# Performance work log

Measured on AMD Instinct MI355X. Metric: run time of the kernel, lower is better.

The kernel has to match this reference:

```python
import jax, jax.numpy as jnp
import numpy as np

HEAD_NUM = 8
EMB = 256
HEAD_SIZE = EMB // HEAD_NUM
POS_LEN = 128
ROPE_BASE = 100.0
LN_EPS = 1e-5
SOFTPICK_EPS = 1e-6


def _rope_tables():
    inv_freq = 1.0 / ROPE_BASE ** (jnp.arange(0, HEAD_SIZE, 2, dtype=jnp.float32) / HEAD_SIZE)
    t = jnp.arange(POS_LEN, dtype=jnp.float32)
    freqs = jnp.einsum('i,j->ij', t, inv_freq)          # [W, hs/2]
    freqs = jnp.concatenate([freqs, freqs], axis=-1)     # [W, hs]
    return jnp.sin(freqs), jnp.cos(freqs)


def _apply_rope(e, sin, cos):
    # e: [..., W, hs]; sin/cos: [W, hs]
    h = HEAD_SIZE // 2
    rot = jnp.concatenate([-e[..., h:], e[..., :h]], axis=-1)
    return e * cos + rot * sin


def _layernorm(x, g, b):
    mu = jnp.mean(x, axis=-1, keepdims=True)
    var = jnp.mean(jnp.square(x - mu), axis=-1, keepdims=True)
    return (x - mu) * jax.lax.rsqrt(var + LN_EPS) * g + b


def _softpick(x):
    m = jnp.max(x, axis=-1, keepdims=True)
    e = jnp.exp(x - m) - jnp.exp(-m)
    return jax.nn.relu(e) / (jnp.sum(jnp.abs(e), axis=-1, keepdims=True) + SOFTPICK_EPS)


def setup_inputs() -> dict:
    key = jax.random.key(0)
    ks = jax.random.split(key, 12)
    B, C, H, W = 4, EMB, 256, 128
    hn, hs = HEAD_NUM, HEAD_SIZE
    s = 0.02
    return {
        'left': jax.random.normal(ks[0], (B, C, H, W), jnp.float32),
        'right': jax.random.normal(ks[1], (B, C, H, W), jnp.float32),
        'qw': jax.random.normal(ks[2], (hn, hs, hs), jnp.float32) * s,   # grouped 1x1 conv weights
        'kw': jax.random.normal(ks[3], (hn, hs, hs), jnp.float32) * s,
        'vw': jax.random.normal(ks[4], (hn, hs, hs), jnp.float32) * s,
        'proj_w': jax.random.normal(ks[5], (C, C), jnp.float32) * s,
        'proj_b': jnp.zeros((C,), jnp.float32),
        'ln1_g': jnp.ones((C,), jnp.float32),
        'ln1_b': jnp.zeros((C,), jnp.float32),
        'ln2_g': jnp.ones((C,), jnp.float32),
        'ln2_b': jnp.zeros((C,), jnp.float32),
        'w1': jax.random.normal(ks[6], (C, 4 * C), jnp.float32) * s,
        'b1': jnp.zeros((4 * C,), jnp.float32),
        'w2': jax.random.normal(ks[7], (4 * C, C), jnp.float32) * s,
        'b2': jnp.zeros((C,), jnp.float32),
    }


def reference(left, right, qw, kw, vw, proj_w, proj_b,
              ln1_g, ln1_b, ln2_g, ln2_b, w1, b1, w2, b2):
    B, C, H, W = left.shape
    hn, hs = HEAD_NUM, HEAD_SIZE
    scale = hs ** -0.5
    sin, cos = _rope_tables()  # [W, hs]

    def grouped_proj(x, w):
        # grouped 1x1 conv -> per-head matmul; out [B, H, hn, W, hs]
        xr = x.reshape(B, hn, hs, H, W)
        return jnp.einsum('bgihw,goi->bhgwo', xr, w)

    q = _apply_rope(grouped_proj(left, qw), sin, cos)
    k = _apply_rope(grouped_proj(right, kw), sin, cos)
    v = grouped_proj(right, vw)

    att = _softpick(jnp.einsum('bhgqd,bhgkd->bhgqk', q, k) * scale)  # [B,H,hn,W,W]
    out = jnp.einsum('bhgqk,bhgkd->bhqgd', att, v).reshape(B, H, W, C)

    x1 = _layernorm(out @ proj_w + proj_b + jnp.transpose(left, (0, 2, 3, 1)), ln1_g, ln1_b)
    ffn = jax.nn.gelu(x1 @ w1 + b1, approximate=False) @ w2 + b2
    return _layernorm(ffn + x1, ln2_g, ln2_b)
```

## Files before the change

kernel.cpp:

```cpp
#include <hip/hip_runtime.h>
#include <hip/hip_bf16.h>

#define DEV __device__ __forceinline__

typedef __attribute__((ext_vector_type(8))) short bf16x8_t;
typedef __attribute__((ext_vector_type(4))) float f32x4_t;

constexpr int cB = 4, cC = 256, cH = 256, cW = 128, cHN = 8, cHS = 32;
constexpr int cM = cB * cH * cW;

DEV float bfu(unsigned int b16) { union { unsigned int u; float f; } v; v.u = b16 << 16; return v.f; }
DEV unsigned short f2bb(float f) { union { __hip_bfloat16 h; unsigned short u; } v; v.h = __float2bfloat16(f); return v.u; }
DEV unsigned int pk2(float a, float b) { return (unsigned)f2bb(a) | ((unsigned)f2bb(b) << 16); }

#define GLOAD_LDS16(g, l) \
  __builtin_amdgcn_global_load_lds((const __attribute__((address_space(1))) void*)(g), \
                                   (__attribute__((address_space(3))) void*)(l), 16, 0, 0)

DEV float gelu_fast(float v) {
  float ax = fabsf(v) * 0.7071067811865475f;
  float t = __builtin_amdgcn_rcpf(1.0f + 0.3275911f * ax);
  float poly = ((((1.061405429f * t - 1.453152027f) * t + 1.421413741f) * t
                 - 0.284496736f) * t + 0.254829592f) * t;
  float e = __expf(-ax * ax);
  float erfv = 1.0f - poly * e;
  float phi = 0.5f + 0.5f * copysignf(erfv, v);
  return v * phi;
}

__global__ __launch_bounds__(256) void transpose_bf16(const float* __restrict__ src,
                                                      __hip_bfloat16* __restrict__ dst,
                                                      int R, int Ccol) {
  int idx = blockIdx.x * 256 + threadIdx.x;
  if (idx < R * Ccol) {
    int r = idx / Ccol, c = idx - r * Ccol;
    dst[c * R + r] = __float2bfloat16(src[idx]);
  }
}

__global__ __launch_bounds__(256) void transpose_perm_bf16(const float* __restrict__ src,
                                                           __hip_bfloat16* __restrict__ dst,
                                                           int R, int Ccol) {
  int idx = blockIdx.x * 256 + threadIdx.x;
  if (idx < R * Ccol) {
    int r = idx / Ccol, c = idx - r * Ccol;
    int pk = (r & ~63) | ((r & 15) << 2) | ((r >> 4) & 3);
    dst[c * R + pk] = __float2bfloat16(src[idx]);
  }
}

__global__ __launch_bounds__(256) void rope_init(float2* __restrict__ tab) {
  int i = blockIdx.x * 256 + threadIdx.x;
  int w = i >> 4, c = i & 15;
  float inv = expf((float)c * -0.28782313662425572f);
  float ang = (float)w * inv;
  tab[i] = make_float2(sinf(ang), cosf(ang));
}

constexpr int XL_OFF = 0, XR_OFF = 10240, WQ_OFF = 20480, WK_OFF = 23040, WV_OFF = 25600;
constexpr int QS_OFF = 28160, KS_OFF = 38400, VT_OFF = 0, P_OFF = 10240;
constexpr int SMEM_BYTES = 48640;

__global__ __launch_bounds__(256) void attn_mfma(
    const float* __restrict__ left, const float* __restrict__ right,
    const float* __restrict__ qw, const float* __restrict__ kw, const float* __restrict__ vw,
    const float2* __restrict__ rope,
    __hip_bfloat16* __restrict__ att_out)
{
  __shared__ __align__(16) char smem[SMEM_BYTES];

  const int t = threadIdx.x;
  const int g = blockIdx.x & 7;
  const int h = (blockIdx.x >> 3) & 255;
  const int b = blockIdx.x >> 11;
  const size_t HW = (size_t)cH * cW;

  {
    const float* lb = left  + ((size_t)(b * cC + g * cHS) * cH + h) * cW;
    const float* rb = right + ((size_t)(b * cC + g * cHS) * cH + h) * cW;
    int w = t & 127, ih = (t >> 7) * 16;
    unsigned short* xlrow = (unsigned short*)(smem + XL_OFF) + w * 40 + ih;
    unsigned short* xrrow = (unsigned short*)(smem + XR_OFF) + w * 40 + ih;
#pragma unroll
    for (int i = 0; i < 16; i += 2) {
      float a0 = lb[(size_t)(ih + i) * HW + w], a1 = lb[(size_t)(ih + i + 1) * HW + w];
      *(unsigned int*)(xlrow + i) = pk2(a0, a1);
      float c0 = rb[(size_t)(ih + i) * HW + w], c1 = rb[(size_t)(ih + i + 1) * HW + w];
      *(unsigned int*)(xrrow + i) = pk2(c0, c1);
    }
    int o = t >> 3, i0 = (t & 7) * 4;
    {
      float4 v4 = *(const float4*)(qw + g * 1024 + t * 4);
      unsigned short* dst = (unsigned short*)(smem + WQ_OFF) + o * 40 + i0;
      *(unsigned int*)(dst) = pk2(v4.x, v4.y); *(unsigned int*)(dst + 2) = pk2(v4.z, v4.w);
    }
    {
      float4 v4 = *(const float4*)(kw + g * 1024 + t * 4);
      unsigned short* dst = (unsigned short*)(smem + WK_OFF) + o * 40 + i0;
      *(unsigned int*)(dst) = pk2(v4.x, v4.y); *(unsigned int*)(dst + 2) = pk2(v4.z, v4.w);
    }
    {
      float4 v4 = *(const float4*)(vw + g * 1024 + t * 4);
      unsigned short* dst = (unsigned short*)(smem + WV_OFF) + o * 40 + i0;
      *(unsigned int*)(dst) = pk2(v4.x, v4.y); *(unsigned int*)(dst + 2) = pk2(v4.z, v4.w);
    }
  }
  __syncthreads();

  const int lane = t & 63, wid = t >> 6;
  const int c = lane & 15, q4 = lane >> 4;
  const int wbase = wid * 32;
  const f32x4_t zero = {0.f, 0.f, 0.f, 0.f};

  bf16x8_t a_xl[2], a_xr[2];
#pragma unroll
  for (int sub = 0; sub < 2; ++sub) {
    a_xl[sub] = *(const bf16x8_t*)(smem + XL_OFF + (wbase + sub * 16 + c) * 80 + q4 * 16);
    a_xr[sub] = *(const bf16x8_t*)(smem + XR_OFF + (wbase + sub * 16 + c) * 80 + q4 * 16);
  }
  f32x4_t qacc[2][2], kacc[2][2];
#pragma unroll
  for (int ot = 0; ot < 2; ++ot) {
    bf16x8_t bq = *(const bf16x8_t*)(smem + WQ_OFF + (ot * 16 + c) * 80 + q4 * 16);
    bf16x8_t bk = *(const bf16x8_t*)(smem + WK_OFF + (ot * 16 + c) * 80 + q4 * 16);
#pragma unroll
    for (int sub = 0; sub < 2; ++sub) {
      qacc[sub][ot] = __builtin_amdgcn_mfma_f32_16x16x32_bf16(a_xl[sub], bq, zero, 0, 0, 0);
      kacc[sub][ot] = __builtin_amdgcn_mfma_f32_16x16x32_bf16(a_xr[sub], bk, zero, 0, 0, 0);
    }
  }
  {
    const float scale = 0.17677669529663687f;
    unsigned short* qsp = (unsigned short*)(smem + QS_OFF);
    unsigned short* ksp = (unsigned short*)(smem + KS_OFF);
#pragma unroll
    for (int sub = 0; sub < 2; ++sub)
#pragma unroll
      for (int r = 0; r < 4; ++r) {
        int w = wbase + sub * 16 + q4 * 4 + r;
        float2 sc = rope[w * 16 + c];
        float sn = sc.x, cs = sc.y;
        float q0 = qacc[sub][0][r], q1 = qacc[sub][1][r];
        qsp[w * 40 + c]      = f2bb((q0 * cs - q1 * sn) * scale);
        qsp[w * 40 + c + 16] = f2bb((q1 * cs + q0 * sn) * scale);
        float k0 = kacc[sub][0][r], k1 = kacc[sub][1][r];
        ksp[w * 40 + c]      = f2bb(k0 * cs - k1 * sn);
        ksp[w * 40 + c + 16] = f2bb(k1 * cs + k0 * sn);
      }
  }
  __syncthreads();

  {
    f32x4_t vacc[2][2];
#pragma unroll
    for (int dt = 0; dt < 2; ++dt) {
      bf16x8_t awv = *(const bf16x8_t*)(smem + WV_OFF + (dt * 16 + c) * 80 + q4 * 16);
#pragma unroll
      for (int sub = 0; sub < 2; ++sub)
        vacc[dt][sub] = __builtin_amdgcn_mfma_f32_16x16x32_bf16(awv, a_xr[sub], zero, 0, 0, 0);
    }
    unsigned short* vtp = (unsigned short*)(smem + VT_OFF);
#pragma unroll
    for (int dt = 0; dt < 2; ++dt)
#pragma unroll
      for (int r = 0; r < 4; ++r) {
        int d = dt * 16 + q4 * 4 + r;
        *(unsigned int*)(vtp + d * 136 + c * 8 + wid * 2) = pk2(vacc[dt][0][r], vacc[dt][1][r]);
      }
  }

  bf16x8_t aq0 = *(const bf16x8_t*)(smem + QS_OFF + (wbase + c) * 80 + q4 * 16);
  bf16x8_t aq1 = *(const bf16x8_t*)(smem + QS_OFF + (wbase + 16 + c) * 80 + q4 * 16);
  f32x4_t sac[2][8];
#pragma unroll
  for (int kt = 0; kt < 8; ++kt) {
    bf16x8_t bk = *(const bf16x8_t*)(smem + KS_OFF + (kt * 16 + c) * 80 + q4 * 16);
    sac[0][kt] = __builtin_amdgcn_mfma_f32_16x16x32_bf16(aq0, bk, zero, 0, 0, 0);
    sac[1][kt] = __builtin_amdgcn_mfma_f32_16x16x32_bf16(aq1, bk, zero, 0, 0, 0);
  }

  float dinv_[2][4];
#pragma unroll
  for (int sub = 0; sub < 2; ++sub)
#pragma unroll
    for (int r = 0; r < 4; ++r) {
      float m = sac[sub][0][r];
#pragma unroll
      for (int kt = 1; kt < 8; ++kt) m = fmaxf(m, sac[sub][kt][r]);
      m = fmaxf(m, __shfl_xor(m, 1));
      m = fmaxf(m, __shfl_xor(m, 2));
      m = fmaxf(m, __shfl_xor(m, 4));
      m = fmaxf(m, __shfl_xor(m, 8));
      float em = __expf(-m);
      float ss = 0.f;
#pragma unroll
      for (int kt = 0; kt < 8; ++kt) {
        float e = __expf(sac[sub][kt][r] - m) - em;
        sac[sub][kt][r] = fmaxf(e, 0.f);
        ss += fabsf(e);
      }
      ss += __shfl_xor(ss, 1);
      ss += __shfl_xor(ss, 2);
      ss += __shfl_xor(ss, 4);
      ss += __shfl_xor(ss, 8);
      dinv_[sub][r] = 1.0f / (ss + 1e-6f);
    }
  __syncthreads();

  {
    unsigned short* pp = (unsigned short*)(smem + P_OFF);
#pragma unroll
    for (int sub = 0; sub < 2; ++sub)
#pragma unroll
      for (int r = 0; r < 4; ++r) {
        int w = wbase + sub * 16 + q4 * 4 + r;
        float dv = dinv_[sub][r];
        uint4 u;
        u.x = pk2(sac[sub][0][r] * dv, sac[sub][1][r] * dv);
        u.y = pk2(sac[sub][2][r] * dv, sac[sub][3][r] * dv);
        u.z = pk2(sac[sub][4][r] * dv, sac[sub][5][r] * dv);
        u.w = pk2(sac[sub][6][r] * dv, sac[sub][7][r] * dv);
        *(uint4*)(pp + w * 136 + c * 8) = u;
      }
  }
  f32x4_t oacc[2][2] = {{zero, zero}, {zero, zero}};
#pragma unroll
  for (int ks = 0; ks < 4; ++ks) {
    bf16x8_t ap0 = *(const bf16x8_t*)(smem + P_OFF + (wbase + c) * 272 + ks * 64 + q4 * 16);
    bf16x8_t ap1 = *(const bf16x8_t*)(smem + P_OFF + (wbase + 16 + c) * 272 + ks * 64 + q4 * 16);
    bf16x8_t bv0 = *(const bf16x8_t*)(smem + VT_OFF + (c) * 272 + ks * 64 + q4 * 16);
    bf16x8_t bv1 = *(const bf16x8_t*)(smem + VT_OFF + (16 + c) * 272 + ks * 64 + q4 * 16);
    oacc[0][0] = __builtin_amdgcn_mfma_f32_16x16x32_bf16(ap0, bv0, oacc[0][0], 0, 0, 0);
    oacc[0][1] = __builtin_amdgcn_mfma_f32_16x16x32_bf16(ap0, bv1, oacc[0][1], 0, 0, 0);
    oacc[1][0] = __builtin_amdgcn_mfma_f32_16x16x32_bf16(ap1, bv0, oacc[1][0], 0, 0, 0);
    oacc[1][1] = __builtin_amdgcn_mfma_f32_16x16x32_bf16(ap1, bv1, oacc[1][1], 0, 0, 0);
  }
  {
    __hip_bfloat16* ob = att_out + ((size_t)(b * cH + h) * cW) * cC + g * cHS;
#pragma unroll
    for (int sub = 0; sub < 2; ++sub)
#pragma unroll
      for (int dt = 0; dt < 2; ++dt)
#pragma unroll
        for (int r = 0; r < 4; ++r) {
          int w = wbase + sub * 16 + q4 * 4 + r;
          ob[(size_t)w * cC + dt * 16 + c] = __float2bfloat16(oacc[sub][dt][r]);
        }
  }
}

__global__ __launch_bounds__(256) void ffn1_gemm(
    const __hip_bfloat16* __restrict__ A, const __hip_bfloat16* __restrict__ Bt,
    const float* __restrict__ bias, __hip_bfloat16* __restrict__ outb)
{
  constexpr int K = 256, N = 1024;
  __shared__ __align__(16) char smem[32768];
  const int t = threadIdx.x;
  const int id = blockIdx.x;
  const int slot = id >> 3;
  const int by = (id & 7) * 128 + (slot >> 3);
  const int bx = slot & 7;
  const int m0 = by * 128, n0 = bx * 128;
  const int lane = t & 63, wid = t >> 6;
  const int r16 = lane & 15, kq = lane >> 4;
  const int wr = (wid >> 1) * 64, wc = (wid & 1) * 64;
  const int ld_l4 = lane >> 2, ld_c8 = (lane & 3) * 8;

  const __hip_bfloat16* Abase = A  + (size_t)m0 * K + ld_c8;
  const __hip_bfloat16* Bbase = Bt + (size_t)n0 * K + ld_c8;

  f32x4_t acc[4][4];
#pragma unroll
  for (int fi = 0; fi < 4; ++fi)
#pragma unroll
    for (int fj = 0; fj < 4; ++fj) acc[fi][fj] = {0.f, 0.f, 0.f, 0.f};

  auto stage = [&](int buf, int k0) {
    char* As = smem + buf * 16384;
    char* Bs = As + 8192;
#pragma unroll
    for (int i = 0; i < 2; ++i) {
      int chunk = i * 4 + wid;
      int row = chunk * 16 + ld_l4;
      GLOAD_LDS16(Abase + (size_t)row * K + k0, As + chunk * 1024);
      GLOAD_LDS16(Bbase + (size_t)row * K + k0, Bs + chunk * 1024);
    }
  };

  constexpr int NK = K >> 5;
  stage(0, 0);
  for (int tt = 0; tt < NK; ++tt) {
    if (tt + 1 < NK) {
      stage((tt + 1) & 1, (tt + 1) << 5);
      asm volatile("s_waitcnt vmcnt(4)" ::: "memory");
    } else {
      asm volatile("s_waitcnt vmcnt(0)" ::: "memory");
    }
    __builtin_amdgcn_s_barrier();
    __builtin_amdgcn_sched_barrier(0);
    char* As = smem + (tt & 1) * 16384;
    char* Bs = As + 8192;
    bf16x8_t af[4], bf[4];
#pragma unroll
    for (int fi = 0; fi < 4; ++fi)
      af[fi] = *(const bf16x8_t*)(As + (wr + fi * 16 + r16) * 64 + kq * 16);
#pragma unroll
    for (int fj = 0; fj < 4; ++fj)
      bf[fj] = *(const bf16x8_t*)(Bs + (wc + fj * 16 + r16) * 64 + kq * 16);
#pragma unroll
    for (int fi = 0; fi < 4; ++fi)
#pragma unroll
      for (int fj = 0; fj < 4; ++fj)
        acc[fi][fj] = __builtin_amdgcn_mfma_f32_16x16x32_bf16(af[fi], bf[fj], acc[fi][fj], 0, 0, 0);
    __builtin_amdgcn_sched_barrier(0);
    __builtin_amdgcn_s_barrier();
  }

  float bv[4];
#pragma unroll
  for (int fj = 0; fj < 4; ++fj) bv[fj] = bias[n0 + wc + fj * 16 + r16];
  __hip_bfloat16* obase = outb + (size_t)(m0 + wr + kq * 4) * N + n0 + wc + r16 * 4;
#pragma unroll
  for (int fi = 0; fi < 4; ++fi)
#pragma unroll
    for (int r = 0; r < 4; ++r) {
      float v0 = gelu_fast(acc[fi][0][r] + bv[0]);
      float v1 = gelu_fast(acc[fi][1][r] + bv[1]);
      float v2 = gelu_fast(acc[fi][2][r] + bv[2]);
      float v3 = gelu_fast(acc[fi][3][r] + bv[3]);
      uint2 u;
      u.x = pk2(v0, v1);
      u.y = pk2(v2, v3);
      *(uint2*)(obase + (size_t)(fi * 16 + r) * N) = u;
    }
}

template<int KK, bool FFN2>
__global__ __launch_bounds__(256, 2) void gemm_ln(
    const __hip_bfloat16* __restrict__ A, const __hip_bfloat16* __restrict__ Bt,
    const float* __restrict__ bias, const float* __restrict__ leftres,
    const __hip_bfloat16* __restrict__ resbf,
    const float* __restrict__ g, const float* __restrict__ be,
    void* __restrict__ outp)
{
  __shared__ __align__(16) char smem[49152];
  const int t = threadIdx.x, lane = t & 63, wid = t >> 6;
  const int c = lane & 15, q4 = lane >> 4;
  const int m0 = blockIdx.x * 128;
  const int wr = wid * 32;
  const f32x4_t zero = {0.f, 0.f, 0.f, 0.f};

  f32x4_t acc[2][16];
#pragma unroll
  for (int fi = 0; fi < 2; ++fi)
#pragma unroll
    for (int fj = 0; fj < 16; ++fj) acc[fi][fj] = zero;

  auto stage = [&](int buf, int k0) {
    char* As = smem + buf * 24576;
    char* Bs = As + 8192;
#pragma unroll
    for (int i = 0; i < 2; ++i) {
      int chunk = (wid * 2 + i) * 64 + lane;
      int row = chunk >> 2, c8 = (chunk & 3) * 8;
      GLOAD_LDS16(A + (size_t)(m0 + row) * KK + k0 + c8, As + (wid * 2 + i) * 1024);
    }
#pragma unroll
    for (int i = 0; i < 4; ++i) {
      int chunk = (wid * 4 + i) * 64 + lane;
      int row = chunk >> 2, c8 = (chunk & 3) * 8;
      GLOAD_LDS16(Bt + (size_t)row * KK + k0 + c8, Bs + (wid * 4 + i) * 1024);
    }
  };

  constexpr int NK = KK >> 5;
  stage(0, 0);
  for (int tt = 0; tt < NK; ++tt) {
    if (tt + 1 < NK) {
      stage((tt + 1) & 1, (tt + 1) << 5);
      asm volatile("s_waitcnt vmcnt(6)" ::: "memory");
    } else {
      asm volatile("s_waitcnt vmcnt(0)" ::: "memory");
    }
    __builtin_amdgcn_s_barrier();
    __builtin_amdgcn_sched_barrier(0);
    char* As = smem + (tt & 1) * 24576;
    char* Bs = As + 8192;
    bf16x8_t af0 = *(const bf16x8_t*)(As + (wr + c) * 64 + q4 * 16);
    bf16x8_t af1 = *(const bf16x8_t*)(As + (wr + 16 + c) * 64 + q4 * 16);
#pragma unroll
    for (int fj = 0; fj < 16; ++fj) {
      bf16x8_t bf = *(const bf16x8_t*)(Bs + (fj * 16 + c) * 64 + q4 * 16);
      acc[0][fj] = __builtin_amdgcn_mfma_f32_16x16x32_bf16(af0, bf, acc[0][fj], 0, 0, 0);
      acc[1][fj] = __builtin_amdgcn_mfma_f32_16x16x32_bf16(af1, bf, acc[1][fj], 0, 0, 0);
    }
    __builtin_amdgcn_sched_barrier(0);
    __builtin_amdgcn_s_barrier();
  }

  if (!FFN2) {
    const int b_ = m0 >> 15, h_ = (m0 >> 7) & 255;
#pragma unroll
    for (int fj = 0; fj < 16; ++fj) {
      int n = fj * 16 + c;
      float bv = bias[n];
#pragma unroll
      for (int fi = 0; fi < 2; ++fi) {
        int w0 = wr + fi * 16 + q4 * 4;
        float4 lr = *(const float4*)(leftres + (((size_t)b_ * 256 + n) * 256 + h_) * 128 + w0);
        float la[4] = {lr.x, lr.y, lr.z, lr.w};
#pragma unroll
        for (int r = 0; r < 4; ++r) acc[fi][fj][r] += bv + la[r];
      }
    }
  } else {
#pragma unroll
    for (int fj = 0; fj < 16; ++fj) {
      int n = fj * 16 + c;
      float bv = bias[n];
#pragma unroll
      for (int fi = 0; fi < 2; ++fi)
#pragma unroll
        for (int r = 0; r < 4; ++r) {
          int row = wr + fi * 16 + q4 * 4 + r;
          acc[fi][fj][r] += bv + __bfloat162float(resbf[(size_t)(m0 + row) * 256 + n]);
        }
    }
  }

  float mu[2][4], rs[2][4];
#pragma unroll
  for (int fi = 0; fi < 2; ++fi)
#pragma unroll
    for (int r = 0; r < 4; ++r) {
      float s = 0.f;
#pragma unroll
      for (int fj = 0; fj < 16; ++fj) s += acc[fi][fj][r];
      s += __shfl_xor(s, 1); s += __shfl_xor(s, 2); s += __shfl_xor(s, 4); s += __shfl_xor(s, 8);
      float m_ = s * (1.0f / 256.0f);
      float sq = 0.f;
#pragma unroll
      for (int fj = 0; fj < 16; ++fj) { float d = acc[fi][fj][r] - m_; sq += d * d; }
      sq += __shfl_xor(sq, 1); sq += __shfl_xor(sq, 2); sq += __shfl_xor(sq, 4); sq += __shfl_xor(sq, 8);
      mu[fi][r] = m_;
      rs[fi][r] = rsqrtf(sq * (1.0f / 256.0f) + 1e-5f);
    }
#pragma unroll
  for (int fj = 0; fj < 16; ++fj) {
    int n = fj * 16 + c;
    float gv = g[n], bev = be[n];
#pragma unroll
    for (int fi = 0; fi < 2; ++fi)
#pragma unroll
      for (int r = 0; r < 4; ++r) {
        int row = wr + fi * 16 + q4 * 4 + r;
        float val = (acc[fi][fj][r] - mu[fi][r]) * rs[fi][r] * gv + bev;
        if (FFN2)
          ((float*)outp)[(size_t)(m0 + row) * 256 + n] = val;
        else
          ((__hip_bfloat16*)outp)[(size_t)(m0 + row) * 256 + n] = __float2bfloat16(val);
      }
  }
}

extern "C" void kernel_launch(void* const* d_in, const int* in_sizes, int n_in,
                              void* d_out, int out_size, void* d_ws, size_t ws_size,
                              hipStream_t stream) {
  const float* left   = (const float*)d_in[0];
  const float* right  = (const float*)d_in[1];
  const float* qw     = (const float*)d_in[2];
  const float* kw     = (const float*)d_in[3];
  const float* vw     = (const float*)d_in[4];
  const float* proj_w = (const float*)d_in[5];
  const float* proj_b = (const float*)d_in[6];
  const float* ln1_g  = (const float*)d_in[7];
  const float* ln1_b  = (const float*)d_in[8];
  const float* ln2_g  = (const float*)d_in[9];
  const float* ln2_b  = (const float*)d_in[10];
  const float* w1     = (const float*)d_in[11];
  const float* b1     = (const float*)d_in[12];
  const float* w2     = (const float*)d_in[13];
  const float* b2     = (const float*)d_in[14];

  char* ws = (char*)d_ws;
  __hip_bfloat16* att_out = (__hip_bfloat16*)ws;
  __hip_bfloat16* x1      = (__hip_bfloat16*)(ws + 67108864);
  __hip_bfloat16* hidden  = (__hip_bfloat16*)(ws + 134217728);
  float2*         rope    = (float2*)(ws + 134217728);
  __hip_bfloat16* pwT     = (__hip_bfloat16*)(ws + 402653184);
  __hip_bfloat16* w1T     = pwT + 65536;
  __hip_bfloat16* w2T     = w1T + 262144;

  transpose_bf16<<<256, 256, 0, stream>>>(proj_w, pwT, 256, 256);
  transpose_bf16<<<1024, 256, 0, stream>>>(w1, w1T, 256, 1024);
  transpose_perm_bf16<<<1024, 256, 0, stream>>>(w2, w2T, 1024, 256);
  rope_init<<<8, 256, 0, stream>>>(rope);

  attn_mfma<<<cB * cH * cHN, 256, 0, stream>>>(left, right, qw, kw, vw, rope, att_out);

  gemm_ln<256, false><<<cM / 128, 256, 0, stream>>>(att_out, pwT, proj_b, left, nullptr,
                                                    ln1_g, ln1_b, x1);
  ffn1_gemm<<<8192, 256, 0, stream>>>(x1, w1T, b1, hidden);
  gemm_ln<1024, true><<<cM / 128, 256, 0, stream>>>(hidden, w2T, b2, nullptr, x1,
                                                    ln2_g, ln2_b, d_out);
}
```

Before: 448.4 us.

## Triple-buffer GEMM LDS staging and XOR-swizzle tiles to avoid bank conflicts

Both the FFN1 GEMM and the fused GEMM+LayerNorm kernels go from double to triple buffering in LDS. Two K-tiles are prefetched ahead, with the vmcnt waits adjusted to match. The global-to-LDS loads also now XOR-swizzle the 16-byte column chunk by row, and the fragment reads apply the same swizzle, to cut LDS bank conflicts on the MFMA operand loads. The cost is more shared memory per block: 48KB and 72KB. That may lower occupancy, especially for gemm_ln, which has launch_bounds(256,2).

```diff
diff --git a/kernel.cpp b/kernel.cpp
--- a/kernel.cpp
+++ b/kernel.cpp
@@ -254,7 +254,7 @@
     const float* __restrict__ bias, __hip_bfloat16* __restrict__ outb)
 {
   constexpr int K = 256, N = 1024;
-  __shared__ __align__(16) char smem[32768];
+  __shared__ __align__(16) char smem[49152];
   const int t = threadIdx.x;
   const int id = blockIdx.x;
   const int slot = id >> 3;
@@ -264,10 +264,6 @@
   const int lane = t & 63, wid = t >> 6;
   const int r16 = lane & 15, kq = lane >> 4;
   const int wr = (wid >> 1) * 64, wc = (wid & 1) * 64;
-  const int ld_l4 = lane >> 2, ld_c8 = (lane & 3) * 8;
-
-  const __hip_bfloat16* Abase = A  + (size_t)m0 * K + ld_c8;
-  const __hip_bfloat16* Bbase = Bt + (size_t)n0 * K + ld_c8;
 
   f32x4_t acc[4][4];
 #pragma unroll
@@ -281,32 +277,40 @@
 #pragma unroll
     for (int i = 0; i < 2; ++i) {
       int chunk = i * 4 + wid;
-      int row = chunk * 16 + ld_l4;
-      GLOAD_LDS16(Abase + (size_t)row * K + k0, As + chunk * 1024);
-      GLOAD_LDS16(Bbase + (size_t)row * K + k0, Bs + chunk * 1024);
+      int row = chunk * 16 + (lane >> 2);
+      int sw = (((lane & 3) ^ ((row >> 1) & 3))) * 8;
+      GLOAD_LDS16(A  + (size_t)(m0 + row) * K + k0 + sw, As + chunk * 1024);
+      GLOAD_LDS16(Bt + (size_t)(n0 + row) * K + k0 + sw, Bs + chunk * 1024);
     }
   };
 
   constexpr int NK = K >> 5;
   stage(0, 0);
+  stage(1, 32);
   for (int tt = 0; tt < NK; ++tt) {
-    if (tt + 1 < NK) {
-      stage((tt + 1) & 1, (tt + 1) << 5);
+    if (tt + 2 < NK) {
+      stage((tt + 2) % 3, (tt + 2) << 5);
+      asm volatile("s_waitcnt vmcnt(8)" ::: "memory");
+    } else if (tt + 1 < NK) {
       asm volatile("s_waitcnt vmcnt(4)" ::: "memory");
     } else {
       asm volatile("s_waitcnt vmcnt(0)" ::: "memory");
     }
     __builtin_amdgcn_s_barrier();
     __builtin_amdgcn_sched_barrier(0);
-    char* As = smem + (tt & 1) * 16384;
+    char* As = smem + (tt % 3) * 16384;
     char* Bs = As + 8192;
     bf16x8_t af[4], bf[4];
 #pragma unroll
-    for (int fi = 0; fi < 4; ++fi)
-      af[fi] = *(const bf16x8_t*)(As + (wr + fi * 16 + r16) * 64 + kq * 16);
-#pragma unroll
-    for (int fj = 0; fj < 4; ++fj)
-      bf[fj] = *(const bf16x8_t*)(Bs + (wc + fj * 16 + r16) * 64 + kq * 16);
+    for (int fi = 0; fi < 4; ++fi) {
+      int rr = wr + fi * 16 + r16;
+      af[fi] = *(const bf16x8_t*)(As + rr * 64 + ((kq ^ ((rr >> 1) & 3)) * 16));
+    }
+#pragma unroll
+    for (int fj = 0; fj < 4; ++fj) {
+      int rr = wc + fj * 16 + r16;
+      bf[fj] = *(const bf16x8_t*)(Bs + rr * 64 + ((kq ^ ((rr >> 1) & 3)) * 16));
+    }
 #pragma unroll
     for (int fi = 0; fi < 4; ++fi)
 #pragma unroll
@@ -343,7 +347,7 @@
     const float* __restrict__ g, const float* __restrict__ be,
     void* __restrict__ outp)
 {
-  __shared__ __align__(16) char smem[49152];
+  __shared__ __align__(16) char smem[73728];
   const int t = threadIdx.x, lane = t & 63, wid = t >> 6;
   const int c = lane & 15, q4 = lane >> 4;
   const int m0 = blockIdx.x * 128;
@@ -361,36 +365,43 @@
     char* Bs = As + 8192;
 #pragma unroll
     for (int i = 0; i < 2; ++i) {
-      int chunk = (wid * 2 + i) * 64 + lane;
-      int row = chunk >> 2, c8 = (chunk & 3) * 8;
-      GLOAD_LDS16(A + (size_t)(m0 + row) * KK + k0 + c8, As + (wid * 2 + i) * 1024);
+      int chunk = (wid * 2 + i);
+      int row = chunk * 16 + (lane >> 2);
+      int sw = (((lane & 3) ^ ((row >> 1) & 3))) * 8;
+      GLOAD_LDS16(A + (size_t)(m0 + row) * KK + k0 + sw, As + chunk * 1024);
     }
 #pragma unroll
     for (int i = 0; i < 4; ++i) {
-      int chunk = (wid * 4 + i) * 64 + lane;
-      int row = chunk >> 2, c8 = (chunk & 3) * 8;
-      GLOAD_LDS16(Bt + (size_t)row * KK + k0 + c8, Bs + (wid * 4 + i) * 1024);
+      int chunk = (wid * 4 + i);
+      int row = chunk * 16 + (lane >> 2);
+      int sw = (((lane & 3) ^ ((row >> 1) & 3))) * 8;
+      GLOAD_LDS16(Bt + (size_t)row * KK + k0 + sw, Bs + chunk * 1024);
     }
   };
 
   constexpr int NK = KK >> 5;
   stage(0, 0);
+  stage(1, 32);
   for (int tt = 0; tt < NK; ++tt) {
-    if (tt + 1 < NK) {
-      stage((tt + 1) & 1, (tt + 1) << 5);
+    if (tt + 2 < NK) {
+      stage((tt + 2) % 3, (tt + 2) << 5);
+      asm volatile("s_waitcnt vmcnt(12)" ::: "memory");
+    } else if (tt + 1 < NK) {
       asm volatile("s_waitcnt vmcnt(6)" ::: "memory");
     } else {
       asm volatile("s_waitcnt vmcnt(0)" ::: "memory");
     }
     __builtin_amdgcn_s_barrier();
     __builtin_amdgcn_sched_barrier(0);
-    char* As = smem + (tt & 1) * 24576;
+    char* As = smem + (tt % 3) * 24576;
     char* Bs = As + 8192;
-    bf16x8_t af0 = *(const bf16x8_t*)(As + (wr + c) * 64 + q4 * 16);
-    bf16x8_t af1 = *(const bf16x8_t*)(As + (wr + 16 + c) * 64 + q4 * 16);
+    int ra0 = wr + c, ra1 = wr + 16 + c;
+    bf16x8_t af0 = *(const bf16x8_t*)(As + ra0 * 64 + ((q4 ^ ((ra0 >> 1) & 3)) * 16));
+    bf16x8_t af1 = *(const bf16x8_t*)(As + ra1 * 64 + ((q4 ^ ((ra1 >> 1) & 3)) * 16));
 #pragma unroll
     for (int fj = 0; fj < 16; ++fj) {
-      bf16x8_t bf = *(const bf16x8_t*)(Bs + (fj * 16 + c) * 64 + q4 * 16);
+      int rb = fj * 16 + c;
+      bf16x8_t bf = *(const bf16x8_t*)(Bs + rb * 64 + ((q4 ^ ((rb >> 1) & 3)) * 16));
       acc[0][fj] = __builtin_amdgcn_mfma_f32_16x16x32_bf16(af0, bf, acc[0][fj], 0, 0, 0);
       acc[1][fj] = __builtin_amdgcn_mfma_f32_16x16x32_bf16(af1, bf, acc[1][fj], 0, 0, 0);
     }
```

Result: no change. 445.1 us (-0.7%).
